# Kernel optimization log

Hardware: AMD Instinct MI355X
Metric: run time of the kernel (lower is better)

The kernel has to match this reference:

```python
import jax, jax.numpy as jnp
import numpy as np


def exp_segsum(x):
    """exp(segsum(x)) with the -inf mask folded into a zero mask (same math).
    x: (..., T) -> (..., T, T) lower-triangular decay matrix."""
    T = x.shape[-1]
    xr = jnp.broadcast_to(x[..., None], (*x.shape, T))  # (..., d, e) = x[..., d]
    lower = jnp.tril(jnp.ones((T, T), dtype=bool), -1)
    seg = jnp.cumsum(jnp.where(lower, xr, 0.0), axis=-2)
    incl = jnp.tril(jnp.ones((T, T), dtype=bool), 0)
    return jnp.where(incl, jnp.exp(seg), 0.0)


def ssd(x, A, B, C, chunk_size):
    """Mamba2 chunked structured state-space duality.
    x: (b, L, h, p); A: (b, L, h); B, C: (b, L, n) (shared across heads).
    Returns y: (b, L, h, p) and final state (b, h, p, n)."""
    b_, L_, H, P = x.shape
    c = L_ // chunk_size
    xm = x.reshape(b_, c, chunk_size, H, P)                      # b c l h p
    Am = A.reshape(b_, c, chunk_size, H).transpose(0, 3, 1, 2)   # b h c l
    Bm = B.reshape(b_, c, chunk_size, -1)                        # b c l n
    Cm = C.reshape(b_, c, chunk_size, -1)                        # b c l n
    A_cumsum = jnp.cumsum(Am, axis=-1)                           # b h c l
    Lmat = exp_segsum(Am)                                        # b h c l l
    # intra-chunk (diagonal block) outputs
    Y_diag = jnp.einsum('bcln,bcsn,bhcls,bcshp->bclhp', Cm, Bm, Lmat, xm)
    # per-chunk states
    decay_states = jnp.exp(A_cumsum[:, :, :, -1:] - A_cumsum)    # b h c l
    states = jnp.einsum('bcln,bhcl,bclhp->bchpn', Bm, decay_states, xm)
    init = jnp.zeros_like(states[:, :1])
    states = jnp.concatenate([init, states], axis=1)             # b (c+1) h p n
    # inter-chunk recurrence via segsum over chunk-level decays
    decay_chunk = exp_segsum(jnp.pad(A_cumsum[:, :, :, -1], ((0, 0), (0, 0), (1, 0))))
    new_states = jnp.einsum('bhzc,bchpn->bzhpn', decay_chunk, states)
    states, final_state = new_states[:, :-1], new_states[:, -1]
    # state -> output conversion
    decay_out = jnp.exp(A_cumsum)                                # b h c l
    Y_off = jnp.einsum('bcln,bchpn,bhcl->bclhp', Cm, states, decay_out)
    Y = (Y_diag + Y_off).reshape(b_, L_, H, P)
    return Y, final_state


def setup_inputs() -> dict:
    key = jax.random.key(0)
    ks = jax.random.split(key, 4)
    B, L, d_model = 2, 4096, 1024
    expand, head_dim, d_state, d_conv, chunk = 2, 64, 128, 4, 64
    d_inner = d_model * expand           # 2048
    n_heads = d_inner // head_dim        # 32
    d_in_proj = 2 * d_inner + 2 * d_state + n_heads  # 4384
    conv_dim = d_inner + 2 * d_state     # 2304
    x = jax.random.normal(ks[0], (B, L, d_model), jnp.float32)
    in_proj_w = jax.random.normal(ks[1], (d_model, d_in_proj), jnp.float32) / np.sqrt(d_model)
    conv_w = jax.random.normal(ks[2], (d_conv, 1, conv_dim), jnp.float32) * np.sqrt(2.0 / d_conv)
    conv_b = jnp.zeros((conv_dim,), jnp.float32)
    dt_bias = jnp.full((n_heads,), 0.1, jnp.float32)
    A_log = jnp.full((n_heads,), -1.0, jnp.float32)
    D = jnp.full((n_heads,), 0.1, jnp.float32)
    norm_scale = jnp.ones((d_inner,), jnp.float32)
    out_proj_w = jax.random.normal(ks[3], (d_inner, d_model), jnp.float32) / np.sqrt(d_inner)
    return {"x": x, "in_proj_w": in_proj_w, "conv_w": conv_w, "conv_b": conv_b,
            "dt_bias": dt_bias, "A_log": A_log, "D": D, "norm_scale": norm_scale,
            "out_proj_w": out_proj_w, "chunk_size": chunk}


def reference(x, in_proj_w, conv_w, conv_b, dt_bias, A_log, D, norm_scale, out_proj_w, chunk_size):
    n_heads = dt_bias.shape[0]
    d_inner = norm_scale.shape[0]
    head_dim = d_inner // n_heads
    conv_dim = conv_b.shape[0]
    d_state = (conv_dim - d_inner) // 2
    k = conv_w.shape[0]
    A = -jnp.exp(A_log)                                           # (H,)
    zxbcdt = x @ in_proj_w                                        # (B, L, d_in_proj)
    z = zxbcdt[..., :d_inner]
    xbc = zxbcdt[..., d_inner:d_inner + conv_dim]
    dt = jax.nn.softplus(zxbcdt[..., -n_heads:] + dt_bias)       # (B, L, H)
    # causal depthwise conv (pad k-1 both sides then take first L == pad (k-1, 0))
    xbc = jax.lax.conv_general_dilated(
        xbc, conv_w, window_strides=(1,), padding=[(k - 1, 0)],
        dimension_numbers=('NWC', 'WIO', 'NWC'), feature_group_count=conv_dim) + conv_b
    xbc = jax.nn.silu(xbc)
    xs = xbc[..., :d_inner]
    b = xbc[..., d_inner:d_inner + d_state]
    c = xbc[..., d_inner + d_state:]
    xs = xs.reshape(*xs.shape[:2], n_heads, head_dim)            # (B, L, H, P)
    y, ssm_state = ssd(xs * dt[..., None], A * dt, b, c, chunk_size)
    y = y + xs * D[..., None]
    y = y.reshape(*y.shape[:2], d_inner)
    # gated RMSNorm (Mamba2 norm(y, z))
    yz = y * jax.nn.silu(z)
    y = yz * jax.lax.rsqrt(jnp.mean(yz * yz, axis=-1, keepdims=True) + 1e-6) * norm_scale
    return y @ out_proj_w
```

## Files before the change

kernel.cpp:

```cpp
#include <hip/hip_runtime.h>
#include <hip/hip_bf16.h>
#include <math.h>

typedef __hip_bfloat16 bf16;
typedef __attribute__((ext_vector_type(8))) short short8;
typedef __attribute__((ext_vector_type(4))) float f32x4;

constexpr int BB    = 2;
constexpr int LL    = 4096;
constexpr int DM    = 1024;
constexpr int DIN   = 2048;
constexpr int HH    = 32;
constexpr int PP    = 64;
constexpr int NSD   = 128;
constexpr int CONVD = 2304;
constexpr int DPROJ = 4384;
constexpr int NPAD  = 4480;
constexpr int CHK   = 64;
constexpr int NC    = 64;
constexpr int ROWS  = BB * LL;

__device__ __forceinline__ float b2f(bf16 v) { return __bfloat162float(v); }
__device__ __forceinline__ bf16  f2b(float f) { return __float2bfloat16(f); }
__device__ __forceinline__ short f2bs(float f) {
  bf16 b = f2b(f);
  return *reinterpret_cast<short*>(&b);
}
__device__ __forceinline__ void gload16(const short* g, short* l) {
  __builtin_amdgcn_global_load_lds(
      (const __attribute__((address_space(1))) void*)g,
      (__attribute__((address_space(3))) void*)l, 16, 0, 0);
}
template <int N> __device__ __forceinline__ void waitvm() {
  if constexpr (N == 0)      asm volatile("s_waitcnt vmcnt(0)" ::: "memory");
  else if constexpr (N == 3) asm volatile("s_waitcnt vmcnt(3)" ::: "memory");
  else                       asm volatile("s_waitcnt vmcnt(4)" ::: "memory");
}
__device__ __forceinline__ void barrier_raw() {
  asm volatile("s_barrier" ::: "memory");
}

__global__ __launch_bounds__(256) void convert_bf16(const float* __restrict__ in,
                                                    bf16* __restrict__ outp, int n4) {
  int i = blockIdx.x * 256 + threadIdx.x;
  if (i >= n4) return;
  float4 v = *(const float4*)&in[(size_t)i * 4];
  bf16* p = &outp[(size_t)i * 4];
  p[0] = f2b(v.x); p[1] = f2b(v.y); p[2] = f2b(v.z); p[3] = f2b(v.w);
}

__global__ __launch_bounds__(256) void transpose_w(const float* __restrict__ W,
                                                   bf16* __restrict__ Bt,
                                                   int K, int N) {
  __shared__ float Tl[32][33];
  const int n0 = blockIdx.x * 32, k0 = blockIdx.y * 32;
  const int t = threadIdx.x;
  {
    const int kk = t >> 3, nn4 = (t & 7) * 4;
#pragma unroll
    for (int j = 0; j < 4; ++j) {
      int n = n0 + nn4 + j;
      Tl[kk][nn4 + j] = (n < N) ? W[(size_t)(k0 + kk) * N + n] : 0.f;
    }
  }
  __syncthreads();
  {
    const int nn = t >> 3, kk4 = (t & 7) * 4;
#pragma unroll
    for (int j = 0; j < 4; ++j)
      Bt[(size_t)(n0 + nn) * K + k0 + kk4 + j] = f2b(Tl[kk4 + j][nn]);
  }
}

template <int MODE, int MI>
__global__ __launch_bounds__(256) void gemm_mfma(
    const short* __restrict__ A, const short* __restrict__ Bt, int K,
    bf16* __restrict__ zb, bf16* __restrict__ xbcb,
    float* __restrict__ dtraw, float* __restrict__ Cout) {
  constexpr int MROWS = MI * 32;
  constexpr int NL = (MI == 4) ? 4 : 3;
  constexpr int GX = (MODE == 0) ? NPAD / 128 : DM / 128;
  constexpr int GY = (MODE == 0) ? ROWS / 128 : ROWS / 64;
  constexpr int NWG = GX * GY;
  constexpr int CPX = NWG / 8;
  __shared__ short Asl[3][MROWS * 32];
  __shared__ short Bsl[3][128 * 32];
  const int t = threadIdx.x;
  const int l = t & 63;
  const int w = t >> 6;
  const int wr = w >> 1, wc = w & 1;

  int bid = blockIdx.y * GX + blockIdx.x;
  bid = (bid & 7) * CPX + (bid >> 3);
  const int m0 = (bid / GX) * MROWS;
  const int n0 = (bid % GX) * 128;

  const int srow = l >> 2;
  const int sk   = (((l & 3) - ((l >> 3) & 3)) & 3) * 8;
  const short* gA0 = &A [(size_t)(m0 + w * 16 + srow) * K + sk];
  const short* gA1 = (MI == 4) ? &A[(size_t)(m0 + (4 + w) * 16 + srow) * K + sk]
                               : gA0;
  const short* gB0 = &Bt[(size_t)(n0 + w * 16 + srow) * K + sk];
  const short* gB1 = &Bt[(size_t)(n0 + (4 + w) * 16 + srow) * K + sk];
  const int ldsW0 = (w * 16) * 32, ldsW1 = ((4 + w) * 16) * 32;

  auto STAGE = [&](int buf) {
    gload16(gA0, &Asl[buf][ldsW0]);
    if constexpr (MI == 4) gload16(gA1, &Asl[buf][ldsW1]);
    gload16(gB0, &Bsl[buf][ldsW0]);
    gload16(gB1, &Bsl[buf][ldsW1]);
    gA0 += 32; if constexpr (MI == 4) gA1 += 32;
    gB0 += 32; gB1 += 32;
  };

  const int fr = l & 15;
  const int s2 = (((l >> 4) + ((fr >> 1) & 3)) & 3) * 8;
  const int aoff = (wr * (MI * 16) + fr) * 32 + s2;
  const int boff = (wc * 64 + fr) * 32 + s2;

  f32x4 acc[MI][4] = {};
  const int nt = K >> 5;

  STAGE(0);

  for (int ti = 0; ti < nt; ++ti) {
    const int cur = ti % 3;
    if (ti + 1 < nt) {
      STAGE((ti + 1) % 3);
      waitvm<NL>();
    } else {
      waitvm<0>();
    }
    barrier_raw();
    short8 af[MI], bg[4];
#pragma unroll
    for (int i = 0; i < MI; ++i) af[i] = *(const short8*)&Asl[cur][aoff + i * 512];
#pragma unroll
    for (int j = 0; j < 4; ++j)  bg[j] = *(const short8*)&Bsl[cur][boff + j * 512];
#pragma unroll
    for (int i = 0; i < MI; ++i)
#pragma unroll
      for (int j = 0; j < 4; ++j)
        acc[i][j] = __builtin_amdgcn_mfma_f32_16x16x32_bf16(af[i], bg[j],
                                                            acc[i][j], 0, 0, 0);
  }
#pragma unroll
  for (int i = 0; i < MI; ++i) {
#pragma unroll
    for (int j = 0; j < 4; ++j) {
      int gcol = n0 + wc * 64 + j * 16 + (l & 15);
      int grow0 = m0 + wr * (MI * 16) + i * 16 + (l >> 4) * 4;
#pragma unroll
      for (int q = 0; q < 4; ++q) {
        float v = acc[i][j][q];
        int grow = grow0 + q;
        if constexpr (MODE == 0) {
          if (gcol < DIN) {
            zb[(size_t)grow * DIN + gcol] = f2b(v);
          } else if (gcol < DIN + CONVD) {
            xbcb[(size_t)grow * CONVD + (gcol - DIN)] = f2b(v);
          } else if (gcol < DPROJ) {
            dtraw[(size_t)grow * HH + (gcol - DIN - CONVD)] = v;
          }
        } else {
          Cout[(size_t)grow * DM + gcol] = v;
        }
      }
    }
  }
}

__global__ __launch_bounds__(256) void conv_act(
    const bf16* __restrict__ xbc, const float* __restrict__ dtraw,
    const float* __restrict__ convw, const float* __restrict__ convb,
    const float* __restrict__ dtb, const float* __restrict__ alog,
    bf16* __restrict__ xs, bf16* __restrict__ Bb, bf16* __restrict__ Cb,
    float* __restrict__ dtv, float* __restrict__ dtA) {
  const int row = blockIdx.x;
  const int l   = row & (LL - 1);
  const int t   = threadIdx.x;
  if (t < HH) {
    float raw = dtraw[(size_t)row * HH + t] + dtb[t];
    float dt  = (raw > 20.f) ? raw : log1pf(expf(raw));
    dtv[(size_t)row * HH + t] = dt;
    dtA[(size_t)row * HH + t] = -expf(alog[t]) * dt;
  }
  for (int ch = t * 8; ch < CONVD; ch += 2048) {
    float acc[8];
#pragma unroll
    for (int j = 0; j < 8; ++j) acc[j] = convb[ch + j];
#pragma unroll
    for (int k = 0; k < 4; ++k) {
      if (l - 3 + k >= 0) {
        uint4 v = *(const uint4*)&xbc[(size_t)(row - 3 + k) * CONVD + ch];
        const bf16* pv = (const bf16*)&v;
        const float* wp = &convw[k * CONVD + ch];
#pragma unroll
        for (int j = 0; j < 8; ++j) acc[j] += b2f(pv[j]) * wp[j];
      }
    }
    short8 sv;
#pragma unroll
    for (int j = 0; j < 8; ++j) {
      float s = acc[j] / (1.f + expf(-acc[j]));
      sv[j] = f2bs(s);
    }
    if (ch < DIN) {
      *(short8*)&xs[(size_t)row * DIN + ch] = sv;
    } else if (ch < DIN + NSD) {
      *(short8*)&Bb[(size_t)row * NSD + (ch - DIN)] = sv;
    } else {
      *(short8*)&Cb[(size_t)row * NSD + (ch - DIN - NSD)] = sv;
    }
  }
}

__global__ __launch_bounds__(256) void gmat(const bf16* __restrict__ Bb,
                                            const bf16* __restrict__ Cb,
                                            float* __restrict__ G) {
  const int c = blockIdx.x, b = blockIdx.y;
  const int row0 = (b * NC + c) * CHK;
  __shared__ short Csh[64][136];
  __shared__ short Bsh[64][136];
  const int t = threadIdx.x;
  const int lane = t & 63, w = t >> 6;
#pragma unroll
  for (int i = 0; i < 4; ++i) {
    int f = t + i * 256;
    int rr = f >> 4, n0 = (f & 15) * 8;
    *(uint4*)&Csh[rr][n0] = *(const uint4*)&Cb[(size_t)(row0 + rr) * NSD + n0];
    *(uint4*)&Bsh[rr][n0] = *(const uint4*)&Bb[(size_t)(row0 + rr) * NSD + n0];
  }
  __syncthreads();
  f32x4 acc[4] = {};
  const int r = lane & 15, hi = lane >> 4;
#pragma unroll
  for (int kk = 0; kk < 4; ++kk) {
    short8 af = *(const short8*)&Csh[16 * w + r][kk * 32 + hi * 8];
#pragma unroll
    for (int j = 0; j < 4; ++j) {
      short8 bg = *(const short8*)&Bsh[16 * j + r][kk * 32 + hi * 8];
      acc[j] = __builtin_amdgcn_mfma_f32_16x16x32_bf16(af, bg, acc[j], 0, 0, 0);
    }
  }
#pragma unroll
  for (int j = 0; j < 4; ++j)
#pragma unroll
    for (int q = 0; q < 4; ++q) {
      int ll = 16 * w + hi * 4 + q, ss = 16 * j + r;
      G[((size_t)(b * NC + c) * CHK + ll) * CHK + ss] = acc[j][q];
    }
}

__global__ __launch_bounds__(256) void ssd_chunk(
    const float* __restrict__ G, const bf16* __restrict__ xsp,
    const bf16* __restrict__ Bb, const float* __restrict__ dtv,
    const float* __restrict__ dtA,
    bf16* __restrict__ y, bf16* __restrict__ states, float* __restrict__ cumA) {
  const int h = blockIdx.x, c = blockIdx.y, b = blockIdx.z;
  const int row0 = (b * NC + c) * CHK;
  __shared__ short GMb[64][72];
  __shared__ short xdsT[64][72];
  __shared__ short BdT[128][72];
  __shared__ float cA[CHK], dec[CHK], sdt[CHK];
  const int t = threadIdx.x;
  const int lane = t & 63, w = t >> 6;
  if (t < CHK) {
    sdt[t] = dtv[(size_t)(row0 + t) * HH + h];
    float v = dtA[(size_t)(row0 + t) * HH + h];
#pragma unroll
    for (int o = 1; o < 64; o <<= 1) {
      float u = __shfl_up(v, o, 64);
      if (t >= o) v += u;
    }
    cA[t] = v;
  }
  __syncthreads();
  if (t < CHK) {
    dec[t] = expf(cA[CHK - 1] - cA[t]);
    cumA[((size_t)(b * HH + h) * NC + c) * CHK + t] = cA[t];
  }
#pragma unroll
  for (int i = 0; i < 2; ++i) {
    int f = t + i * 256;
    int ll = f >> 3, p0 = (f & 7) * 8;
    uint4 v = *(const uint4*)&xsp[(size_t)(row0 + ll) * DIN + h * PP + p0];
    const bf16* pv = (const bf16*)&v;
    float dtl = sdt[ll];
#pragma unroll
    for (int j = 0; j < 8; ++j) xdsT[p0 + j][ll] = f2bs(b2f(pv[j]) * dtl);
  }
#pragma unroll
  for (int i = 0; i < 4; ++i) {
    int f = t + i * 256;
    int ll = f >> 4, s0 = (f & 15) * 4;
    float4 g = *(const float4*)&G[((size_t)(b * NC + c) * CHK + ll) * CHK + s0];
    float ca = cA[ll];
    GMb[ll][s0 + 0] = f2bs((s0 + 0 <= ll) ? g.x * expf(ca - cA[s0 + 0]) : 0.f);
    GMb[ll][s0 + 1] = f2bs((s0 + 1 <= ll) ? g.y * expf(ca - cA[s0 + 1]) : 0.f);
    GMb[ll][s0 + 2] = f2bs((s0 + 2 <= ll) ? g.z * expf(ca - cA[s0 + 2]) : 0.f);
    GMb[ll][s0 + 3] = f2bs((s0 + 3 <= ll) ? g.w * expf(ca - cA[s0 + 3]) : 0.f);
  }
  __syncthreads();
#pragma unroll
  for (int i = 0; i < 4; ++i) {
    int f = t + i * 256;
    int ll = f >> 4, n0 = (f & 15) * 8;
    uint4 v = *(const uint4*)&Bb[(size_t)(row0 + ll) * NSD + n0];
    const bf16* pv = (const bf16*)&v;
    float dl = dec[ll];
#pragma unroll
    for (int j = 0; j < 8; ++j) BdT[n0 + j][ll] = f2bs(b2f(pv[j]) * dl);
  }
  __syncthreads();
  const int r = lane & 15, hi = lane >> 4;
  {
    f32x4 acc[4] = {};
#pragma unroll
    for (int kk = 0; kk < 2; ++kk) {
      short8 af = *(const short8*)&GMb[16 * w + r][kk * 32 + hi * 8];
#pragma unroll
      for (int j = 0; j < 4; ++j) {
        short8 bg = *(const short8*)&xdsT[16 * j + r][kk * 32 + hi * 8];
        acc[j] = __builtin_amdgcn_mfma_f32_16x16x32_bf16(af, bg, acc[j], 0, 0, 0);
      }
    }
#pragma unroll
    for (int j = 0; j < 4; ++j)
#pragma unroll
      for (int q = 0; q < 4; ++q) {
        int ll = 16 * w + hi * 4 + q, pp = 16 * j + r;
        y[(size_t)(row0 + ll) * DIN + h * PP + pp] = f2b(acc[j][q]);
      }
  }
  {
    f32x4 acc[8] = {};
#pragma unroll
    for (int kk = 0; kk < 2; ++kk) {
      short8 af = *(const short8*)&xdsT[16 * w + r][kk * 32 + hi * 8];
#pragma unroll
      for (int j = 0; j < 8; ++j) {
        short8 bg = *(const short8*)&BdT[16 * j + r][kk * 32 + hi * 8];
        acc[j] = __builtin_amdgcn_mfma_f32_16x16x32_bf16(af, bg, acc[j], 0, 0, 0);
      }
    }
    size_t sb = ((size_t)(b * NC + c) * HH + h) * (PP * NSD);
#pragma unroll
    for (int j = 0; j < 8; ++j)
#pragma unroll
      for (int q = 0; q < 4; ++q) {
        int pp = 16 * w + hi * 4 + q, nn = 16 * j + r;
        states[sb + (size_t)pp * NSD + nn] = f2b(acc[j][q]);
      }
  }
}

__global__ __launch_bounds__(256) void scan(bf16* __restrict__ states,
                                            const float* __restrict__ cumA) {
  const int q = blockIdx.x, h = blockIdx.y, b = blockIdx.z;
  const int t = threadIdx.x;
  const int off = q * 2048 + t * 8;
  const size_t cstride = (size_t)HH * PP * NSD;
  size_t base = ((size_t)(b * NC) * HH + h) * (PP * NSD) + off;
  const float* cp = &cumA[(size_t)(b * HH + h) * NC * CHK + CHK - 1];
  float S[8] = {};
  uint4 nv = *(const uint4*)&states[base];
  for (int c = 0; c < NC; ++c) {
    uint4 cv = nv;
    if (c + 1 < NC) nv = *(const uint4*)&states[base + cstride];
    float tot = expf(cp[(size_t)c * CHK]);
    const bf16* pin = (const bf16*)&cv;
    short8 sv;
#pragma unroll
    for (int i = 0; i < 8; ++i) {
      float cs = b2f(pin[i]);
      sv[i] = f2bs(S[i]);
      S[i] = S[i] * tot + cs;
    }
    *(short8*)&states[base] = sv;
    base += cstride;
  }
}

__global__ __launch_bounds__(256) void yoff(
    const bf16* __restrict__ Cb, const bf16* __restrict__ states,
    const float* __restrict__ cumA, const bf16* __restrict__ xs,
    const float* __restrict__ Dp, bf16* __restrict__ y) {
  const int h = blockIdx.x, c = blockIdx.y, b = blockIdx.z;
  const int row0 = (b * NC + c) * CHK;
  __shared__ short Csh[64][136];
  __shared__ short Ssh[64][136];
  __shared__ float dcy[CHK];
  const int t = threadIdx.x;
  const int lane = t & 63, w = t >> 6;
  if (t < CHK) dcy[t] = expf(cumA[((size_t)(b * HH + h) * NC + c) * CHK + t]);
  const size_t sbase = ((size_t)(b * NC + c) * HH + h) * (PP * NSD);
#pragma unroll
  for (int i = 0; i < 4; ++i) {
    int f = t + i * 256;
    int rr = f >> 4, n0 = (f & 15) * 8;
    *(uint4*)&Csh[rr][n0] = *(const uint4*)&Cb[(size_t)(row0 + rr) * NSD + n0];
    *(uint4*)&Ssh[rr][n0] = *(const uint4*)&states[sbase + (size_t)rr * NSD + n0];
  }
  __syncthreads();
  f32x4 acc[4] = {};
  const int r = lane & 15, hi = lane >> 4;
#pragma unroll
  for (int kk = 0; kk < 4; ++kk) {
    short8 af = *(const short8*)&Csh[16 * w + r][kk * 32 + hi * 8];
#pragma unroll
    for (int j = 0; j < 4; ++j) {
      short8 bg = *(const short8*)&Ssh[16 * j + r][kk * 32 + hi * 8];
      acc[j] = __builtin_amdgcn_mfma_f32_16x16x32_bf16(af, bg, acc[j], 0, 0, 0);
    }
  }
  const float Dh = Dp[h];
#pragma unroll
  for (int j = 0; j < 4; ++j)
#pragma unroll
    for (int q = 0; q < 4; ++q) {
      int ll = 16 * w + hi * 4 + q, pp = 16 * j + r;
      size_t idx = (size_t)(row0 + ll) * DIN + h * PP + pp;
      y[idx] = f2b(b2f(y[idx]) + acc[j][q] * dcy[ll] + b2f(xs[idx]) * Dh);
    }
}

__global__ __launch_bounds__(256) void gatenorm(const bf16* __restrict__ y,
                                                const bf16* __restrict__ zb,
                                                const float* __restrict__ nsc,
                                                bf16* __restrict__ outn) {
  const int row = blockIdx.x, t = threadIdx.x;
  const int ch = t * 8;
  uint4 yv4 = *(const uint4*)&y [(size_t)row * DIN + ch];
  uint4 zv4 = *(const uint4*)&zb[(size_t)row * DIN + ch];
  const bf16* yp = (const bf16*)&yv4;
  const bf16* zp = (const bf16*)&zv4;
  float v[8];
  float ss = 0.f;
#pragma unroll
  for (int i = 0; i < 8; ++i) {
    float z  = b2f(zp[i]);
    float g  = b2f(yp[i]) * z / (1.f + expf(-z));
    v[i] = g;
    ss += g * g;
  }
#pragma unroll
  for (int off = 32; off > 0; off >>= 1) ss += __shfl_down(ss, off, 64);
  __shared__ float red[4];
  if ((t & 63) == 0) red[t >> 6] = ss;
  __syncthreads();
  float tot = red[0] + red[1] + red[2] + red[3];
  float r = rsqrtf(tot * (1.f / DIN) + 1e-6f);
  short8 o;
#pragma unroll
  for (int i = 0; i < 8; ++i) o[i] = f2bs(v[i] * r * nsc[ch + i]);
  *(short8*)&outn[(size_t)row * DIN + ch] = o;
}

extern "C" void kernel_launch(void* const* d_in, const int* in_sizes, int n_in,
                              void* d_out, int out_size, void* d_ws, size_t ws_size,
                              hipStream_t stream) {
  const float* x     = (const float*)d_in[0];
  const float* inw   = (const float*)d_in[1];
  const float* convw = (const float*)d_in[2];
  const float* convb = (const float*)d_in[3];
  const float* dtb   = (const float*)d_in[4];
  const float* alog  = (const float*)d_in[5];
  const float* Dp    = (const float*)d_in[6];
  const float* nsc   = (const float*)d_in[7];
  const float* outw  = (const float*)d_in[8];
  float* out = (float*)d_out;

  char* p = (char*)d_ws;
  bf16*  zb     = (bf16*)p;  p += (size_t)ROWS * DIN * 2;
  bf16*  xbcb   = (bf16*)p;  p += (size_t)ROWS * CONVD * 2;
  bf16*  y      = xbcb;
  float* dtraw  = (float*)p; p += (size_t)ROWS * HH * 4;
  bf16*  xs     = (bf16*)p;  p += (size_t)ROWS * DIN * 2;
  bf16*  states = (bf16*)p;  p += (size_t)BB * NC * HH * PP * NSD * 2;
  bf16*  normb  = states;
  bf16*  Bb     = (bf16*)p;  p += (size_t)ROWS * NSD * 2;
  bf16*  Cb     = (bf16*)p;  p += (size_t)ROWS * NSD * 2;
  float* dtv    = (float*)p; p += (size_t)ROWS * HH * 4;
  float* dtA    = (float*)p; p += (size_t)ROWS * HH * 4;
  float* cumA   = (float*)p; p += (size_t)BB * HH * NC * CHK * 4;
  float* G      = (float*)p; p += (size_t)BB * NC * CHK * CHK * 4;
  bf16*  xb     = (bf16*)p;  p += (size_t)ROWS * DM * 2;
  bf16*  BtIn   = (bf16*)p;  p += (size_t)NPAD * DM * 2;
  bf16*  BtOut  = xb;

  convert_bf16<<<(ROWS * DM / 4 + 255) / 256, 256, 0, stream>>>(x, xb, ROWS * DM / 4);
  transpose_w<<<dim3(NPAD / 32, DM / 32), 256, 0, stream>>>(inw, BtIn, DM, DPROJ);
  gemm_mfma<0, 4><<<dim3(NPAD / 128, ROWS / 128), 256, 0, stream>>>(
      (const short*)xb, (const short*)BtIn, DM, zb, xbcb, dtraw, nullptr);
  transpose_w<<<dim3(DM / 32, DIN / 32), 256, 0, stream>>>(outw, BtOut, DIN, DM);
  conv_act<<<ROWS, 256, 0, stream>>>(xbcb, dtraw, convw, convb, dtb, alog,
                                     xs, Bb, Cb, dtv, dtA);
  gmat<<<dim3(NC, BB), 256, 0, stream>>>(Bb, Cb, G);
  ssd_chunk<<<dim3(HH, NC, BB), 256, 0, stream>>>(G, xs, Bb, dtv, dtA,
                                                  y, states, cumA);
  scan<<<dim3(4, HH, BB), 256, 0, stream>>>(states, cumA);
  yoff<<<dim3(HH, NC, BB), 256, 0, stream>>>(Cb, states, cumA, xs, Dp, y);
  gatenorm<<<ROWS, 256, 0, stream>>>(y, zb, nsc, normb);
  gemm_mfma<1, 2><<<dim3(DM / 128, ROWS / 64), 256, 0, stream>>>(
      (const short*)normb, (const short*)BtOut, DIN, nullptr, nullptr, nullptr, out);

  (void)in_sizes; (void)n_in; (void)out_size; (void)ws_size;
}
```

Baseline: 347.6 us.

## Replace in-projection GEMM with 256x256-tile 8-wave pipelined MFMA kernel

The input projection GEMM moves from 128x128 tiles with 4 waves to 256x256 tiles with 8 waves and BK=64. It double-buffers in 128KB of dynamic LDS, interleaves half-tile global loads with four MFMA phases, and raises wave priority around the MFMA bursts. The aim is more data reuse per load and better overlap of loads with matrix math on the largest GEMM. In exchange, N padding grows to 4608, so more columns are wasted, and the larger tile gives fewer workgroups (18x32), which risks an imbalanced last wave. The output GEMM is only specialized into its own kernel.

```diff
diff --git a/kernel.cpp b/kernel.cpp
--- a/kernel.cpp
+++ b/kernel.cpp
@@ -15,10 +15,15 @@
 constexpr int NSD   = 128;
 constexpr int CONVD = 2304;
 constexpr int DPROJ = 4384;
-constexpr int NPAD  = 4480;
 constexpr int CHK   = 64;
 constexpr int NC    = 64;
 constexpr int ROWS  = BB * LL;
+
+constexpr int NPAD2 = 4608;
+constexpr int GX2   = NPAD2 / 256;
+constexpr int GY2   = ROWS / 256;
+constexpr int NWG2  = GX2 * GY2;
+constexpr int NT2   = DM / 64;
 
 __device__ __forceinline__ float b2f(bf16 v) { return __bfloat162float(v); }
 __device__ __forceinline__ bf16  f2b(float f) { return __float2bfloat16(f); }
@@ -72,18 +77,157 @@
   }
 }
 
-template <int MODE, int MI>
-__global__ __launch_bounds__(256) void gemm_mfma(
-    const short* __restrict__ A, const short* __restrict__ Bt, int K,
-    bf16* __restrict__ zb, bf16* __restrict__ xbcb,
-    float* __restrict__ dtraw, float* __restrict__ Cout) {
-  constexpr int MROWS = MI * 32;
-  constexpr int NL = (MI == 4) ? 4 : 3;
-  constexpr int GX = (MODE == 0) ? NPAD / 128 : DM / 128;
-  constexpr int GY = (MODE == 0) ? ROWS / 128 : ROWS / 64;
-  constexpr int NWG = GX * GY;
-  constexpr int CPX = NWG / 8;
-  __shared__ short Asl[3][MROWS * 32];
+__global__ __launch_bounds__(512, 2) void gemm256_inproj(
+    const short* __restrict__ A, const short* __restrict__ Bt,
+    bf16* __restrict__ zb, bf16* __restrict__ xbcb, float* __restrict__ dtraw) {
+  extern __shared__ short smem[];
+  short* AslS = smem;
+  short* BslS = smem + 2 * 256 * 64;
+  const int t = threadIdx.x;
+  const int l = t & 63;
+  const int wid = t >> 6;
+  const int wr = wid >> 2, wc = wid & 3;
+
+  int bid = blockIdx.y * GX2 + blockIdx.x;
+  bid = (bid & 7) * (NWG2 / 8) + (bid >> 3);
+  const int m0 = (bid / GX2) * 256;
+  const int n0 = (bid % GX2) * 256;
+
+  const int srow  = l >> 3;
+  const int sslot = ((l & 7) - srow) & 7;
+  const short* gAl = A  + (size_t)(m0 + srow) * DM + sslot * 8;
+  const short* gBl = Bt + (size_t)(n0 + srow) * DM + sslot * 8;
+
+  const int fr = l & 15, hi = l >> 4;
+
+  f32x4 acc[8][4] = {};
+  short8 afr[4][2], bfr[4][2];
+
+  auto stageA = [&](int kt, int h) {
+    const int buf = kt & 1;
+#pragma unroll
+    for (int q = 0; q < 2; ++q) {
+      int rbase = h * 128 + (wid * 2 + q) * 8;
+      gload16(gAl + (size_t)rbase * DM + kt * 64,
+              AslS + buf * (256 * 64) + rbase * 64);
+    }
+  };
+  auto stageB = [&](int kt, int h) {
+    const int buf = kt & 1;
+#pragma unroll
+    for (int q = 0; q < 2; ++q) {
+      int rbase = h * 128 + (wid * 2 + q) * 8;
+      gload16(gBl + (size_t)rbase * DM + kt * 64,
+              BslS + buf * (256 * 64) + rbase * 64);
+    }
+  };
+  auto rdA = [&](int kt, int i, int ks) -> short8 {
+    int row = wr * 128 + i * 16 + fr;
+    int ps  = ((ks * 4 + hi) + (fr & 7)) & 7;
+    return *(const short8*)&AslS[(kt & 1) * (256 * 64) + row * 64 + ps * 8];
+  };
+  auto rdB = [&](int kt, int j, int ks) -> short8 {
+    int row = wc * 64 + j * 16 + fr;
+    int ps  = ((ks * 4 + hi) + (fr & 7)) & 7;
+    return *(const short8*)&BslS[(kt & 1) * (256 * 64) + row * 64 + ps * 8];
+  };
+
+  stageB(0, 0); stageB(0, 1);
+  stageA(0, 0); stageA(0, 1);
+  stageB(1, 0); stageB(1, 1);
+  waitvm<4>();
+  barrier_raw();
+
+  for (int g = 0; g < NT2; ++g) {
+#pragma unroll
+    for (int i = 0; i < 4; ++i) { afr[i][0] = rdA(g, i, 0); afr[i][1] = rdA(g, i, 1); }
+#pragma unroll
+    for (int j = 0; j < 2; ++j) { bfr[j][0] = rdB(g, j, 0); bfr[j][1] = rdB(g, j, 1); }
+    if (g + 1 < NT2) stageA(g + 1, 0);
+    barrier_raw();
+    __builtin_amdgcn_s_setprio(1);
+#pragma unroll
+    for (int i = 0; i < 4; ++i)
+#pragma unroll
+      for (int j = 0; j < 2; ++j) {
+        acc[i][j] = __builtin_amdgcn_mfma_f32_16x16x32_bf16(afr[i][0], bfr[j][0], acc[i][j], 0, 0, 0);
+        acc[i][j] = __builtin_amdgcn_mfma_f32_16x16x32_bf16(afr[i][1], bfr[j][1], acc[i][j], 0, 0, 0);
+      }
+    __builtin_amdgcn_s_setprio(0);
+    barrier_raw();
+#pragma unroll
+    for (int j = 2; j < 4; ++j) { bfr[j][0] = rdB(g, j, 0); bfr[j][1] = rdB(g, j, 1); }
+    if (g + 1 < NT2) stageA(g + 1, 1);
+    barrier_raw();
+    __builtin_amdgcn_s_setprio(1);
+#pragma unroll
+    for (int i = 0; i < 4; ++i)
+#pragma unroll
+      for (int j = 2; j < 4; ++j) {
+        acc[i][j] = __builtin_amdgcn_mfma_f32_16x16x32_bf16(afr[i][0], bfr[j][0], acc[i][j], 0, 0, 0);
+        acc[i][j] = __builtin_amdgcn_mfma_f32_16x16x32_bf16(afr[i][1], bfr[j][1], acc[i][j], 0, 0, 0);
+      }
+    __builtin_amdgcn_s_setprio(0);
+    barrier_raw();
+#pragma unroll
+    for (int i = 0; i < 4; ++i) { afr[i][0] = rdA(g, 4 + i, 0); afr[i][1] = rdA(g, 4 + i, 1); }
+    if (g + 2 < NT2) stageB(g + 2, 0);
+    barrier_raw();
+    __builtin_amdgcn_s_setprio(1);
+#pragma unroll
+    for (int i = 0; i < 4; ++i)
+#pragma unroll
+      for (int j = 0; j < 2; ++j) {
+        acc[4 + i][j] = __builtin_amdgcn_mfma_f32_16x16x32_bf16(afr[i][0], bfr[j][0], acc[4 + i][j], 0, 0, 0);
+        acc[4 + i][j] = __builtin_amdgcn_mfma_f32_16x16x32_bf16(afr[i][1], bfr[j][1], acc[4 + i][j], 0, 0, 0);
+      }
+    __builtin_amdgcn_s_setprio(0);
+    barrier_raw();
+    if (g + 2 < NT2) stageB(g + 2, 1);
+    if (g + 2 < NT2)      waitvm<4>();
+    else if (g + 1 < NT2) waitvm<0>();
+    barrier_raw();
+    __builtin_amdgcn_s_setprio(1);
+#pragma unroll
+    for (int i = 0; i < 4; ++i)
+#pragma unroll
+      for (int j = 2; j < 4; ++j) {
+        acc[4 + i][j] = __builtin_amdgcn_mfma_f32_16x16x32_bf16(afr[i][0], bfr[j][0], acc[4 + i][j], 0, 0, 0);
+        acc[4 + i][j] = __builtin_amdgcn_mfma_f32_16x16x32_bf16(afr[i][1], bfr[j][1], acc[4 + i][j], 0, 0, 0);
+      }
+    __builtin_amdgcn_s_setprio(0);
+    barrier_raw();
+  }
+
+#pragma unroll
+  for (int i = 0; i < 8; ++i) {
+#pragma unroll
+    for (int j = 0; j < 4; ++j) {
+      int gcol  = n0 + wc * 64 + j * 16 + fr;
+      int grow0 = m0 + wr * 128 + i * 16 + hi * 4;
+#pragma unroll
+      for (int q = 0; q < 4; ++q) {
+        float v = acc[i][j][q];
+        int grow = grow0 + q;
+        if (gcol < DIN) {
+          zb[(size_t)grow * DIN + gcol] = f2b(v);
+        } else if (gcol < DIN + CONVD) {
+          xbcb[(size_t)grow * CONVD + (gcol - DIN)] = f2b(v);
+        } else if (gcol < DPROJ) {
+          dtraw[(size_t)grow * HH + (gcol - DIN - CONVD)] = v;
+        }
+      }
+    }
+  }
+}
+
+__global__ __launch_bounds__(256) void gemm_out(
+    const short* __restrict__ A, const short* __restrict__ Bt,
+    float* __restrict__ Cout) {
+  constexpr int K = DIN;
+  constexpr int GX = DM / 128, GY = ROWS / 64;
+  constexpr int NWG = GX * GY, CPX = NWG / 8;
+  __shared__ short Asl[3][64 * 32];
   __shared__ short Bsl[3][128 * 32];
   const int t = threadIdx.x;
   const int l = t & 63;
@@ -92,82 +236,59 @@
 
   int bid = blockIdx.y * GX + blockIdx.x;
   bid = (bid & 7) * CPX + (bid >> 3);
-  const int m0 = (bid / GX) * MROWS;
+  const int m0 = (bid / GX) * 64;
   const int n0 = (bid % GX) * 128;
 
   const int srow = l >> 2;
   const int sk   = (((l & 3) - ((l >> 3) & 3)) & 3) * 8;
   const short* gA0 = &A [(size_t)(m0 + w * 16 + srow) * K + sk];
-  const short* gA1 = (MI == 4) ? &A[(size_t)(m0 + (4 + w) * 16 + srow) * K + sk]
-                               : gA0;
   const short* gB0 = &Bt[(size_t)(n0 + w * 16 + srow) * K + sk];
   const short* gB1 = &Bt[(size_t)(n0 + (4 + w) * 16 + srow) * K + sk];
   const int ldsW0 = (w * 16) * 32, ldsW1 = ((4 + w) * 16) * 32;
 
   auto STAGE = [&](int buf) {
     gload16(gA0, &Asl[buf][ldsW0]);
-    if constexpr (MI == 4) gload16(gA1, &Asl[buf][ldsW1]);
     gload16(gB0, &Bsl[buf][ldsW0]);
     gload16(gB1, &Bsl[buf][ldsW1]);
-    gA0 += 32; if constexpr (MI == 4) gA1 += 32;
-    gB0 += 32; gB1 += 32;
+    gA0 += 32; gB0 += 32; gB1 += 32;
   };
 
   const int fr = l & 15;
   const int s2 = (((l >> 4) + ((fr >> 1) & 3)) & 3) * 8;
-  const int aoff = (wr * (MI * 16) + fr) * 32 + s2;
+  const int aoff = (wr * 32 + fr) * 32 + s2;
   const int boff = (wc * 64 + fr) * 32 + s2;
 
-  f32x4 acc[MI][4] = {};
+  f32x4 acc[2][4] = {};
   const int nt = K >> 5;
 
   STAGE(0);
-
   for (int ti = 0; ti < nt; ++ti) {
     const int cur = ti % 3;
-    if (ti + 1 < nt) {
-      STAGE((ti + 1) % 3);
-      waitvm<NL>();
-    } else {
-      waitvm<0>();
-    }
-    barrier_raw();
-    short8 af[MI], bg[4];
-#pragma unroll
-    for (int i = 0; i < MI; ++i) af[i] = *(const short8*)&Asl[cur][aoff + i * 512];
-#pragma unroll
-    for (int j = 0; j < 4; ++j)  bg[j] = *(const short8*)&Bsl[cur][boff + j * 512];
-#pragma unroll
-    for (int i = 0; i < MI; ++i)
+    if (ti + 1 < nt) { STAGE((ti + 1) % 3); waitvm<3>(); }
+    else             { waitvm<0>(); }
+    barrier_raw();
+    short8 af[2], bg[4];
+#pragma unroll
+    for (int i = 0; i < 2; ++i) af[i] = *(const short8*)&Asl[cur][aoff + i * 512];
+#pragma unroll
+    for (int j = 0; j < 4; ++j) bg[j] = *(const short8*)&Bsl[cur][boff + j * 512];
+#pragma unroll
+    for (int i = 0; i < 2; ++i)
 #pragma unroll
       for (int j = 0; j < 4; ++j)
         acc[i][j] = __builtin_amdgcn_mfma_f32_16x16x32_bf16(af[i], bg[j],
                                                             acc[i][j], 0, 0, 0);
   }
 #pragma unroll
-  for (int i = 0; i < MI; ++i) {
+  for (int i = 0; i < 2; ++i)
 #pragma unroll
     for (int j = 0; j < 4; ++j) {
       int gcol = n0 + wc * 64 + j * 16 + (l & 15);
-      int grow0 = m0 + wr * (MI * 16) + i * 16 + (l >> 4) * 4;
-#pragma unroll
-      for (int q = 0; q < 4; ++q) {
-        float v = acc[i][j][q];
-        int grow = grow0 + q;
-        if constexpr (MODE == 0) {
-          if (gcol < DIN) {
-            zb[(size_t)grow * DIN + gcol] = f2b(v);
-          } else if (gcol < DIN + CONVD) {
-            xbcb[(size_t)grow * CONVD + (gcol - DIN)] = f2b(v);
-          } else if (gcol < DPROJ) {
-            dtraw[(size_t)grow * HH + (gcol - DIN - CONVD)] = v;
-          }
-        } else {
-          Cout[(size_t)grow * DM + gcol] = v;
-        }
-      }
-    }
-  }
+      int grow0 = m0 + wr * 32 + i * 16 + (l >> 4) * 4;
+#pragma unroll
+      for (int q = 0; q < 4; ++q)
+        Cout[(size_t)(grow0 + q) * DM + gcol] = acc[i][j][q];
+    }
 }
 
 __global__ __launch_bounds__(256) void conv_act(
@@ -486,13 +607,16 @@
   float* cumA   = (float*)p; p += (size_t)BB * HH * NC * CHK * 4;
   float* G      = (float*)p; p += (size_t)BB * NC * CHK * CHK * 4;
   bf16*  xb     = (bf16*)p;  p += (size_t)ROWS * DM * 2;
-  bf16*  BtIn   = (bf16*)p;  p += (size_t)NPAD * DM * 2;
+  bf16*  BtIn   = (bf16*)p;  p += (size_t)NPAD2 * DM * 2;
   bf16*  BtOut  = xb;
 
+  (void)hipFuncSetAttribute((const void*)gemm256_inproj,
+                            hipFuncAttributeMaxDynamicSharedMemorySize, 131072);
+
   convert_bf16<<<(ROWS * DM / 4 + 255) / 256, 256, 0, stream>>>(x, xb, ROWS * DM / 4);
-  transpose_w<<<dim3(NPAD / 32, DM / 32), 256, 0, stream>>>(inw, BtIn, DM, DPROJ);
-  gemm_mfma<0, 4><<<dim3(NPAD / 128, ROWS / 128), 256, 0, stream>>>(
-      (const short*)xb, (const short*)BtIn, DM, zb, xbcb, dtraw, nullptr);
+  transpose_w<<<dim3(NPAD2 / 32, DM / 32), 256, 0, stream>>>(inw, BtIn, DM, DPROJ);
+  gemm256_inproj<<<dim3(GX2, GY2), 512, 131072, stream>>>(
+      (const short*)xb, (const short*)BtIn, zb, xbcb, dtraw);
   transpose_w<<<dim3(DM / 32, DIN / 32), 256, 0, stream>>>(outw, BtOut, DIN, DM);
   conv_act<<<ROWS, 256, 0, stream>>>(xbcb, dtraw, convw, convb, dtb, alog,
                                      xs, Bb, Cb, dtv, dtA);
@@ -502,8 +626,8 @@
   scan<<<dim3(4, HH, BB), 256, 0, stream>>>(states, cumA);
   yoff<<<dim3(HH, NC, BB), 256, 0, stream>>>(Cb, states, cumA, xs, Dp, y);
   gatenorm<<<ROWS, 256, 0, stream>>>(y, zb, nsc, normb);
-  gemm_mfma<1, 2><<<dim3(DM / 128, ROWS / 64), 256, 0, stream>>>(
-      (const short*)normb, (const short*)BtOut, DIN, nullptr, nullptr, nullptr, out);
+  gemm_out<<<dim3(DM / 128, ROWS / 64), 256, 0, stream>>>(
+      (const short*)normb, (const short*)BtOut, out);
 
   (void)in_sizes; (void)n_in; (void)out_size; (void)ws_size;
 }
```

Result: no change. 352.0 us (+1.3%).
